# Optimization experiments

Hardware: AMD Instinct MI355X
Metric: run time of the kernel (lower is better)

Reference implementation:

```python
import jax, jax.numpy as jnp
import numpy as np

BITS = 4
GROUP_SIZE = 128
MAXQ = (1 << BITS) - 1  # 15
PACK = 32 // BITS       # 8 nibbles per int32


def setup_inputs() -> dict:
    key = jax.random.key(0)
    k1, k2, k3, k4, k5 = jax.random.split(key, 5)
    infeatures, outfeatures, tokens = 8192, 8192, 4096
    n_groups = infeatures // GROUP_SIZE  # 64
    x = jax.random.normal(k1, (tokens, infeatures), dtype=jnp.float32)
    qweight = jax.random.randint(k2, (infeatures // PACK, outfeatures), 0, 2147483647, dtype=jnp.int32)
    qzeros = jax.random.randint(k3, (n_groups, outfeatures // PACK), 0, 2147483647, dtype=jnp.int32)
    scales = jax.random.uniform(k4, (n_groups, outfeatures), dtype=jnp.float32) * 0.01 + 0.001
    bias = jax.random.normal(k5, (outfeatures,), dtype=jnp.float32)
    return {"x": x, "qweight": qweight, "qzeros": qzeros, "scales": scales, "bias": bias}


def _dequant(qweight, qzeros, scales):
    shifts = jnp.arange(0, 32, BITS, dtype=jnp.int32)  # [8]
    # unpack weight nibbles: [in/8, 8, out] -> [n_groups, group_size, out]
    w = (qweight[:, None, :] >> shifts[None, :, None]) & MAXQ
    w = w.reshape(-1, GROUP_SIZE, qweight.shape[1])
    # unpack zero points: [ng, out/8, 8] -> [ng, out]; note stored as (zero-1)
    z = ((qzeros[:, :, None] >> shifts[None, None, :]) & MAXQ) + 1
    z = z.reshape(z.shape[0], -1)
    # groupwise dequant: scales * (w - z)
    W = scales[:, None, :] * (w.astype(scales.dtype) - z[:, None, :].astype(scales.dtype))
    return W.reshape(-1, W.shape[-1])  # [infeatures, outfeatures]


def reference(x, qweight, qzeros, scales, bias):
    W = _dequant(qweight, qzeros, scales)
    return x @ W + bias
```

## Files before the change

### kernel.cpp

```cpp
#include <hip/hip_runtime.h>
#include <hip/hip_bf16.h>

constexpr int MM = 4096;
constexpr int NN = 8192;
constexpr int KK = 8192;
constexpr int BM = 256, BN = 256, BK = 64;
constexpr int THREADS = 512;
constexpr int NKB = KK / BK;
constexpr int NT = NN / BN;

typedef __bf16 bf16;
typedef __attribute__((ext_vector_type(8))) __bf16 bf16x8;
typedef __attribute__((ext_vector_type(4))) float floatx4;

__device__ __forceinline__ void async_copy16(const void* g, void* l) {
    __builtin_amdgcn_global_load_lds(
        (const __attribute__((address_space(1))) void*)g,
        (__attribute__((address_space(3))) void*)l, 16, 0, 0);
}

__global__ __launch_bounds__(256)
void convert_x(const float* __restrict__ x, bf16* __restrict__ xb) {
    const int tid = blockIdx.x * 256 + threadIdx.x;
    const int c = tid & 7;
    const int m = (tid >> 3) & 255;
    const int kb = (tid >> 11) & 127;
    const int mtile = tid >> 18;
    const int row = mtile * 256 + m;
    const int col = kb * 64 + c * 8;
    const float4* src = (const float4*)(x + (size_t)row * KK + col);
    const float4 f0 = src[0];
    const float4 f1 = src[1];
    bf16x8 v;
    v[0] = (bf16)f0.x; v[1] = (bf16)f0.y; v[2] = (bf16)f0.z; v[3] = (bf16)f0.w;
    v[4] = (bf16)f1.x; v[5] = (bf16)f1.y; v[6] = (bf16)f1.z; v[7] = (bf16)f1.w;
    const int dst_chunk = (tid & ~7) | (c ^ (m & 7));
    *(bf16x8*)(xb + (size_t)dst_chunk * 8) = v;
}

__global__ __launch_bounds__(THREADS, 2)
void qgemm_dma(const bf16* __restrict__ xb,
               const unsigned* __restrict__ qweight,
               const unsigned* __restrict__ qzeros,
               const float* __restrict__ scales,
               const float* __restrict__ bias,
               float* __restrict__ out)
{
    __shared__ alignas(16) bf16 As[2][BM * BK];
    __shared__ alignas(16) bf16 Bs[2][BN * BK];

    const int t = threadIdx.x;
    const int ntile = blockIdx.x & (NT - 1);
    const int mtile = blockIdx.x / NT;
    const int n0 = ntile * BN;

    const int wave = t >> 6;
    const int lane = t & 63;
    const int wm = (wave >> 1) * 64;
    const int wn = (wave & 1) * 128;
    const int ml = lane & 15;
    const int quad = lane >> 4;

    const int bn = t & 255;
    const int rbase = (t >> 8) * 4;
    const int gn = n0 + bn;

    floatx4 acc[4][8];
#pragma unroll
    for (int i = 0; i < 4; ++i)
#pragma unroll
        for (int j = 0; j < 8; ++j)
            acc[i][j] = (floatx4){0.f, 0.f, 0.f, 0.f};

    const char* xb_base = (const char*)xb
        + (size_t)mtile * NKB * (BM * BK) * sizeof(bf16);

    unsigned bq[4];
    float s = 0.f, sz = 0.f;

    auto stage_a = [&](int kb, int buf) {
        const char* g = xb_base + (size_t)kb * (BM * BK * 2) + wave * 4096 + lane * 16;
        char* l = (char*)&As[buf][0] + wave * 4096;
#pragma unroll
        for (int i = 0; i < 4; ++i)
            async_copy16(g + i * 1024, l + i * 1024);
    };
    auto load_b = [&](int kb) {
#pragma unroll
        for (int i = 0; i < 4; ++i)
            bq[i] = qweight[(size_t)(kb * 8 + rbase + i) * NN + gn];
    };
    auto store_b = [&](int buf) {
#pragma unroll
        for (int i = 0; i < 4; ++i) {
            const int rq = rbase + i;
            bf16x8 v;
#pragma unroll
            for (int j = 0; j < 8; ++j)
                v[j] = (bf16)((float)((bq[i] >> (4 * j)) & 15u) * s - sz);
            *(bf16x8*)&Bs[buf][bn * BK + ((rq ^ (bn & 7)) << 3)] = v;
        }
    };
    auto compute = [&](int buf) {
#pragma unroll
        for (int ks = 0; ks < 2; ++ks) {
            const int clog = ks * 4 + quad;
            bf16x8 af[4];
#pragma unroll
            for (int im = 0; im < 4; ++im) {
                const int row = wm + im * 16 + ml;
                af[im] = *(const bf16x8*)&As[buf][row * BK + ((clog ^ (row & 7)) << 3)];
            }
#pragma unroll
            for (int jh = 0; jh < 2; ++jh) {
                bf16x8 bf4[4];
#pragma unroll
                for (int j = 0; j < 4; ++j) {
                    const int row = wn + (jh * 4 + j) * 16 + ml;
                    bf4[j] = *(const bf16x8*)&Bs[buf][row * BK + ((clog ^ (row & 7)) << 3)];
                }
#pragma unroll
                for (int im = 0; im < 4; ++im)
#pragma unroll
                    for (int j = 0; j < 4; ++j)
                        acc[im][jh * 4 + j] = __builtin_amdgcn_mfma_f32_16x16x32_bf16(
                            af[im], bf4[j], acc[im][jh * 4 + j], 0, 0, 0);
            }
        }
    };

    {
        s = scales[gn];
        const unsigned zw = qzeros[gn >> 3];
        sz = s * (float)(((zw >> (4 * (gn & 7))) & 15u) + 1u);
        stage_a(0, 0);
        load_b(0);
        store_b(0);
    }
    __syncthreads();

    float s_nxt = 0.f;
    unsigned zw_nxt = 0;
    for (int kb = 0; kb < NKB; ++kb) {
        const int p = kb & 1, q = p ^ 1;
        const bool has_next = (kb + 1) < NKB;
        if (has_next) {
            stage_a(kb + 1, q);
            load_b(kb + 1);
            if (((kb + 1) & 1) == 0) {
                const int g = (kb + 1) >> 1;
                s_nxt = scales[(size_t)g * NN + gn];
                zw_nxt = qzeros[(size_t)g * (NN / 8) + (gn >> 3)];
            }
        }
        compute(p);
        if (has_next) {
            if (((kb + 1) & 1) == 0) {
                s = s_nxt;
                sz = s * (float)(((zw_nxt >> (4 * (gn & 7))) & 15u) + 1u);
            }
            store_b(q);
            __syncthreads();
        }
    }

#pragma unroll
    for (int jn = 0; jn < 8; ++jn) {
        const int ngl = n0 + wn + jn * 16 + ml;
        const float bv = bias[ngl];
#pragma unroll
        for (int im = 0; im < 4; ++im) {
            const int mg = mtile * BM + wm + im * 16 + quad * 4;
#pragma unroll
            for (int r = 0; r < 4; ++r)
                out[(size_t)(mg + r) * NN + ngl] = acc[im][jn][r] + bv;
        }
    }
}

__global__ __launch_bounds__(THREADS, 2)
void qgemm_fallback(const float* __restrict__ x,
                    const unsigned* __restrict__ qweight,
                    const unsigned* __restrict__ qzeros,
                    const float* __restrict__ scales,
                    const float* __restrict__ bias,
                    float* __restrict__ out)
{
    __shared__ bf16 As[BM * BK];
    __shared__ bf16 Bs[BN * BK];

    const int t = threadIdx.x;
    const int ntile = blockIdx.x & 31;
    const int mtile = blockIdx.x >> 5;
    const int m0 = mtile * BM;
    const int n0 = ntile * BN;
    const int wave = t >> 6;
    const int lane = t & 63;
    const int wm = (wave >> 1) * 64;
    const int wn = (wave & 1) * 128;
    const int ml = lane & 15;
    const int quad = lane >> 4;
    const int bn = t & 255;
    const int rbase = (t >> 8) * 4;
    const int gn = n0 + bn;

    floatx4 acc[4][8];
    for (int i = 0; i < 4; ++i)
        for (int j = 0; j < 8; ++j)
            acc[i][j] = (floatx4){0.f, 0.f, 0.f, 0.f};

    float s = 0.f, sz = 0.f;

    for (int kb = 0; kb < KK / BK; ++kb) {
        const int k0 = kb * BK;
        if ((kb & 1) == 0) {
            const int g = kb >> 1;
            s = scales[g * NN + gn];
            const unsigned zw = qzeros[g * (NN / 8) + (gn >> 3)];
            const float z = (float)(((zw >> (4 * (gn & 7))) & 15u) + 1u);
            sz = s * z;
        }
#pragma unroll
        for (int i = 0; i < 4; ++i) {
            const int chunk = t + THREADS * i;
            const int m = chunk >> 3;
            const int c = chunk & 7;
            const float4* src = (const float4*)(x + (size_t)(m0 + m) * KK + (k0 + c * 8));
            const float4 f0 = src[0];
            const float4 f1 = src[1];
            bf16x8 v;
            v[0] = (bf16)f0.x; v[1] = (bf16)f0.y; v[2] = (bf16)f0.z; v[3] = (bf16)f0.w;
            v[4] = (bf16)f1.x; v[5] = (bf16)f1.y; v[6] = (bf16)f1.z; v[7] = (bf16)f1.w;
            *(bf16x8*)&As[m * BK + ((c ^ (m & 7)) << 3)] = v;
        }
        const int kq0 = k0 >> 3;
#pragma unroll
        for (int i = 0; i < 4; ++i) {
            const int rq = rbase + i;
            const unsigned q = qweight[(size_t)(kq0 + rq) * NN + gn];
            bf16x8 v;
#pragma unroll
            for (int j = 0; j < 8; ++j) {
                const float f = (float)((q >> (4 * j)) & 15u) * s - sz;
                v[j] = (bf16)f;
            }
            *(bf16x8*)&Bs[bn * BK + ((rq ^ (bn & 7)) << 3)] = v;
        }
        __syncthreads();
#pragma unroll
        for (int ks = 0; ks < 2; ++ks) {
            const int clog = ks * 4 + quad;
            bf16x8 af[4];
            bf16x8 bfr[8];
#pragma unroll
            for (int im = 0; im < 4; ++im) {
                const int row = wm + im * 16 + ml;
                af[im] = *(const bf16x8*)&As[row * BK + ((clog ^ (row & 7)) << 3)];
            }
#pragma unroll
            for (int jn = 0; jn < 8; ++jn) {
                const int row = wn + jn * 16 + ml;
                bfr[jn] = *(const bf16x8*)&Bs[row * BK + ((clog ^ (row & 7)) << 3)];
            }
#pragma unroll
            for (int im = 0; im < 4; ++im)
#pragma unroll
                for (int jn = 0; jn < 8; ++jn)
                    acc[im][jn] = __builtin_amdgcn_mfma_f32_16x16x32_bf16(
                        af[im], bfr[jn], acc[im][jn], 0, 0, 0);
        }
        __syncthreads();
    }
#pragma unroll
    for (int jn = 0; jn < 8; ++jn) {
        const int ngl = n0 + wn + jn * 16 + ml;
        const float bv = bias[ngl];
#pragma unroll
        for (int im = 0; im < 4; ++im) {
            const int mg = m0 + wm + im * 16 + quad * 4;
#pragma unroll
            for (int r = 0; r < 4; ++r)
                out[(size_t)(mg + r) * NN + ngl] = acc[im][jn][r] + bv;
        }
    }
}

extern "C" void kernel_launch(void* const* d_in, const int* in_sizes, int n_in,
                              void* d_out, int out_size, void* d_ws, size_t ws_size,
                              hipStream_t stream) {
    const float*    x       = (const float*)d_in[0];
    const unsigned* qweight = (const unsigned*)d_in[1];
    const unsigned* qzeros  = (const unsigned*)d_in[2];
    const float*    scales  = (const float*)d_in[3];
    const float*    bias    = (const float*)d_in[4];
    float* out = (float*)d_out;

    const int grid = (MM / BM) * (NN / BN);
    const size_t xb_bytes = (size_t)MM * KK * sizeof(bf16);

    if (ws_size >= xb_bytes) {
        bf16* xb = (bf16*)d_ws;
        const int chunks = MM * KK / 8;
        convert_x<<<chunks / 256, 256, 0, stream>>>(x, xb);
        qgemm_dma<<<grid, THREADS, 0, stream>>>(xb, qweight, qzeros, scales, bias, out);
    } else {
        qgemm_fallback<<<grid, THREADS, 0, stream>>>(x, qweight, qzeros, scales, bias, out);
    }
}
```

Measured before the change: 752.1 us.

## Switch main GEMM to 32x32x16 MFMA with fragment-ordered LDS layout

The main kernel moves from 16x16x32 to 32x32x16 bf16 MFMA and halves the block to 256 threads, each wave computing a 128x128 sub-tile. The x conversion kernel and the B dequant store now write data directly in MFMA fragment order, so each lane reads its operand contiguously without an XOR swizzle. The B dequant/store is placed between the k-slices of the compute to overlap with MFMA work. This cuts LDS read traffic per FLOP and instruction count, at the cost of more accumulator registers per thread (256 floats) and a single wave group per CU (launch bounds 1).

```diff
diff --git a/kernel.cpp b/kernel.cpp
--- a/kernel.cpp
+++ b/kernel.cpp
@@ -5,13 +5,14 @@
 constexpr int NN = 8192;
 constexpr int KK = 8192;
 constexpr int BM = 256, BN = 256, BK = 64;
-constexpr int THREADS = 512;
+constexpr int THREADS = 256;
 constexpr int NKB = KK / BK;
 constexpr int NT = NN / BN;
 
 typedef __bf16 bf16;
 typedef __attribute__((ext_vector_type(8))) __bf16 bf16x8;
 typedef __attribute__((ext_vector_type(4))) float floatx4;
+typedef __attribute__((ext_vector_type(16))) float floatx16;
 
 __device__ __forceinline__ void async_copy16(const void* g, void* l) {
     __builtin_amdgcn_global_load_lds(
@@ -21,25 +22,26 @@
 
 __global__ __launch_bounds__(256)
 void convert_x(const float* __restrict__ x, bf16* __restrict__ xb) {
-    const int tid = blockIdx.x * 256 + threadIdx.x;
-    const int c = tid & 7;
-    const int m = (tid >> 3) & 255;
-    const int kb = (tid >> 11) & 127;
-    const int mtile = tid >> 18;
-    const int row = mtile * 256 + m;
-    const int col = kb * 64 + c * 8;
-    const float4* src = (const float4*)(x + (size_t)row * KK + col);
+    const int c = blockIdx.x * 256 + threadIdx.x;
+    const int lane = c & 63;
+    const int ks   = (c >> 6) & 3;
+    const int im   = (c >> 8) & 3;
+    const int wmh  = (c >> 10) & 1;
+    const int kb   = (c >> 11) & 127;
+    const int mt   = c >> 18;
+    const int m = mt * 256 + wmh * 128 + im * 32 + (lane & 31);
+    const int k = kb * 64 + ks * 16 + (lane >> 5) * 8;
+    const float4* src = (const float4*)(x + (size_t)m * KK + k);
     const float4 f0 = src[0];
     const float4 f1 = src[1];
     bf16x8 v;
     v[0] = (bf16)f0.x; v[1] = (bf16)f0.y; v[2] = (bf16)f0.z; v[3] = (bf16)f0.w;
     v[4] = (bf16)f1.x; v[5] = (bf16)f1.y; v[6] = (bf16)f1.z; v[7] = (bf16)f1.w;
-    const int dst_chunk = (tid & ~7) | (c ^ (m & 7));
-    *(bf16x8*)(xb + (size_t)dst_chunk * 8) = v;
-}
-
-__global__ __launch_bounds__(THREADS, 2)
-void qgemm_dma(const bf16* __restrict__ xb,
+    *(bf16x8*)(xb + (size_t)c * 8) = v;
+}
+
+__global__ __launch_bounds__(THREADS, 1)
+void qgemm_big(const bf16* __restrict__ xb,
                const unsigned* __restrict__ qweight,
                const unsigned* __restrict__ qzeros,
                const float* __restrict__ scales,
@@ -56,77 +58,62 @@
 
     const int wave = t >> 6;
     const int lane = t & 63;
-    const int wm = (wave >> 1) * 64;
-    const int wn = (wave & 1) * 128;
-    const int ml = lane & 15;
-    const int quad = lane >> 4;
-
-    const int bn = t & 255;
-    const int rbase = (t >> 8) * 4;
-    const int gn = n0 + bn;
-
-    floatx4 acc[4][8];
+    const int wmh = wave >> 1;
+    const int nfb = (wave & 1) * 4;
+
+    const int nf = t >> 5;
+    const int nl = t & 31;
+    const int gn = n0 + t;
+
+    floatx16 acc[4][4];
 #pragma unroll
     for (int i = 0; i < 4; ++i)
 #pragma unroll
-        for (int j = 0; j < 8; ++j)
-            acc[i][j] = (floatx4){0.f, 0.f, 0.f, 0.f};
-
-    const char* xb_base = (const char*)xb
-        + (size_t)mtile * NKB * (BM * BK) * sizeof(bf16);
-
-    unsigned bq[4];
+        for (int j = 0; j < 4; ++j)
+            acc[i][j] = (floatx16)0.f;
+
+    const char* xb_base = (const char*)xb + (size_t)mtile * NKB * 32768;
+
+    unsigned bq[8];
     float s = 0.f, sz = 0.f;
 
     auto stage_a = [&](int kb, int buf) {
-        const char* g = xb_base + (size_t)kb * (BM * BK * 2) + wave * 4096 + lane * 16;
-        char* l = (char*)&As[buf][0] + wave * 4096;
-#pragma unroll
-        for (int i = 0; i < 4; ++i)
+        const char* g = xb_base + (size_t)kb * 32768 + wave * 8192 + lane * 16;
+        char* l = (char*)&As[buf][0] + wave * 8192;
+#pragma unroll
+        for (int i = 0; i < 8; ++i)
             async_copy16(g + i * 1024, l + i * 1024);
     };
     auto load_b = [&](int kb) {
 #pragma unroll
-        for (int i = 0; i < 4; ++i)
-            bq[i] = qweight[(size_t)(kb * 8 + rbase + i) * NN + gn];
+        for (int r = 0; r < 8; ++r)
+            bq[r] = qweight[(size_t)(kb * 8 + r) * NN + gn];
     };
     auto store_b = [&](int buf) {
 #pragma unroll
-        for (int i = 0; i < 4; ++i) {
-            const int rq = rbase + i;
+        for (int r = 0; r < 8; ++r) {
+            const unsigned q = bq[r];
             bf16x8 v;
 #pragma unroll
             for (int j = 0; j < 8; ++j)
-                v[j] = (bf16)((float)((bq[i] >> (4 * j)) & 15u) * s - sz);
-            *(bf16x8*)&Bs[buf][bn * BK + ((rq ^ (bn & 7)) << 3)] = v;
+                v[j] = (bf16)((float)((q >> (4 * j)) & 15u) * s - sz);
+            *(bf16x8*)&Bs[buf][(((nf * 4 + (r >> 1)) * 64) + (r & 1) * 32 + nl) * 8] = v;
         }
     };
-    auto compute = [&](int buf) {
-#pragma unroll
-        for (int ks = 0; ks < 2; ++ks) {
-            const int clog = ks * 4 + quad;
-            bf16x8 af[4];
-#pragma unroll
-            for (int im = 0; im < 4; ++im) {
-                const int row = wm + im * 16 + ml;
-                af[im] = *(const bf16x8*)&As[buf][row * BK + ((clog ^ (row & 7)) << 3)];
-            }
-#pragma unroll
-            for (int jh = 0; jh < 2; ++jh) {
-                bf16x8 bf4[4];
-#pragma unroll
-                for (int j = 0; j < 4; ++j) {
-                    const int row = wn + (jh * 4 + j) * 16 + ml;
-                    bf4[j] = *(const bf16x8*)&Bs[buf][row * BK + ((clog ^ (row & 7)) << 3)];
-                }
-#pragma unroll
-                for (int im = 0; im < 4; ++im)
-#pragma unroll
-                    for (int j = 0; j < 4; ++j)
-                        acc[im][jh * 4 + j] = __builtin_amdgcn_mfma_f32_16x16x32_bf16(
-                            af[im], bf4[j], acc[im][jh * 4 + j], 0, 0, 0);
-            }
-        }
+    auto compute_ks = [&](int buf, int ks) {
+        bf16x8 af[4], bfr[4];
+#pragma unroll
+        for (int im = 0; im < 4; ++im)
+            af[im] = *(const bf16x8*)&As[buf][(((wmh * 4 + im) * 4 + ks) * 64 + lane) * 8];
+#pragma unroll
+        for (int jn = 0; jn < 4; ++jn)
+            bfr[jn] = *(const bf16x8*)&Bs[buf][(((nfb + jn) * 4 + ks) * 64 + lane) * 8];
+#pragma unroll
+        for (int im = 0; im < 4; ++im)
+#pragma unroll
+            for (int jn = 0; jn < 4; ++jn)
+                acc[im][jn] = __builtin_amdgcn_mfma_f32_32x32x16_bf16(
+                    af[im], bfr[jn], acc[im][jn], 0, 0, 0);
     };
 
     {
@@ -153,32 +140,39 @@
                 zw_nxt = qzeros[(size_t)g * (NN / 8) + (gn >> 3)];
             }
         }
-        compute(p);
+        compute_ks(p, 0);
+        compute_ks(p, 1);
         if (has_next) {
             if (((kb + 1) & 1) == 0) {
                 s = s_nxt;
                 sz = s * (float)(((zw_nxt >> (4 * (gn & 7))) & 15u) + 1u);
             }
             store_b(q);
+        }
+        compute_ks(p, 2);
+        compute_ks(p, 3);
+        if (has_next)
             __syncthreads();
-        }
-    }
-
-#pragma unroll
-    for (int jn = 0; jn < 8; ++jn) {
-        const int ngl = n0 + wn + jn * 16 + ml;
+    }
+
+#pragma unroll
+    for (int jn = 0; jn < 4; ++jn) {
+        const int ngl = n0 + (wave & 1) * 128 + jn * 32 + (lane & 31);
         const float bv = bias[ngl];
 #pragma unroll
         for (int im = 0; im < 4; ++im) {
-            const int mg = mtile * BM + wm + im * 16 + quad * 4;
-#pragma unroll
-            for (int r = 0; r < 4; ++r)
-                out[(size_t)(mg + r) * NN + ngl] = acc[im][jn][r] + bv;
-        }
-    }
-}
-
-__global__ __launch_bounds__(THREADS, 2)
+            const int mbase = mtile * BM + wmh * 128 + im * 32 + 4 * (lane >> 5);
+            const floatx16 a = acc[im][jn];
+#pragma unroll
+            for (int reg = 0; reg < 16; ++reg) {
+                const int mg = mbase + (reg & 3) + 8 * (reg >> 2);
+                out[(size_t)mg * NN + ngl] = a[reg] + bv;
+            }
+        }
+    }
+}
+
+__global__ __launch_bounds__(512, 2)
 void qgemm_fallback(const float* __restrict__ x,
                     const unsigned* __restrict__ qweight,
                     const unsigned* __restrict__ qzeros,
@@ -217,12 +211,11 @@
             const int g = kb >> 1;
             s = scales[g * NN + gn];
             const unsigned zw = qzeros[g * (NN / 8) + (gn >> 3)];
-            const float z = (float)(((zw >> (4 * (gn & 7))) & 15u) + 1u);
-            sz = s * z;
+            sz = s * (float)(((zw >> (4 * (gn & 7))) & 15u) + 1u);
         }
 #pragma unroll
         for (int i = 0; i < 4; ++i) {
-            const int chunk = t + THREADS * i;
+            const int chunk = t + 512 * i;
             const int m = chunk >> 3;
             const int c = chunk & 7;
             const float4* src = (const float4*)(x + (size_t)(m0 + m) * KK + (k0 + c * 8));
@@ -240,10 +233,8 @@
             const unsigned q = qweight[(size_t)(kq0 + rq) * NN + gn];
             bf16x8 v;
 #pragma unroll
-            for (int j = 0; j < 8; ++j) {
-                const float f = (float)((q >> (4 * j)) & 15u) * s - sz;
-                v[j] = (bf16)f;
-            }
+            for (int j = 0; j < 8; ++j)
+                v[j] = (bf16)((float)((q >> (4 * j)) & 15u) * s - sz);
             *(bf16x8*)&Bs[bn * BK + ((rq ^ (bn & 7)) << 3)] = v;
         }
         __syncthreads();
@@ -295,15 +286,16 @@
     const float*    bias    = (const float*)d_in[4];
     float* out = (float*)d_out;
 
-    const int grid = (MM / BM) * (NN / BN);
     const size_t xb_bytes = (size_t)MM * KK * sizeof(bf16);
 
     if (ws_size >= xb_bytes) {
         bf16* xb = (bf16*)d_ws;
         const int chunks = MM * KK / 8;
         convert_x<<<chunks / 256, 256, 0, stream>>>(x, xb);
-        qgemm_dma<<<grid, THREADS, 0, stream>>>(xb, qweight, qzeros, scales, bias, out);
+        const int grid = (MM / BM) * (NN / BN);
+        qgemm_big<<<grid, THREADS, 0, stream>>>(xb, qweight, qzeros, scales, bias, out);
     } else {
-        qgemm_fallback<<<grid, THREADS, 0, stream>>>(x, qweight, qzeros, scales, bias, out);
-    }
-}
+        const int grid = (MM / BM) * (NN / BN);
+        qgemm_fallback<<<grid, 512, 0, stream>>>(x, qweight, qzeros, scales, bias, out);
+    }
+}
```

After: 846.2 us. 1.13x slower.
